# Kernel optimization log

Hardware: AMD Instinct MI355X
Metric: run time of the kernel (lower is better)

The kernel has to match this reference:

```python
import jax, jax.numpy as jnp
import numpy as np


def setup_inputs() -> dict:
    key = jax.random.key(0)
    B, L, C = 32, 1024, 32
    batch_x = jax.random.normal(key, (B, L, C), dtype=jnp.float32)
    return {"batch_x": batch_x, "w": 32}


def reference(batch_x, w):
    # Faithful banded version of dtw_slack: for each timestep t, look at the
    # window [t-w, t+w], compute euclidean distances / n_channels, take the
    # window max, then reduce M = max_t and R2 = sum_t max_t^2 per sample.
    B, L, C = batch_x.shape
    offs = jnp.arange(-w, w + 1)                       # [2w+1]
    t = jnp.arange(L)
    idx = t[:, None] + offs[None, :]                   # [L, 2w+1]
    valid = (idx >= 0) & (idx < L)                     # band edge mask
    idx_c = jnp.clip(idx, 0, L - 1)
    win = batch_x[:, idx_c, :]                         # [B, L, 2w+1, C]
    diff = batch_x[:, :, None, :] - win                # [B, L, 2w+1, C]
    sq = jnp.sum(diff * diff, axis=-1)                 # [B, L, 2w+1]
    # safe sqrt (sqrt(0)=0 exactly, matches torch forward)
    dist = jnp.where(sq > 0, jnp.sqrt(jnp.where(sq > 0, sq, 1.0)), 0.0) / C
    dist = jnp.where(valid[None, :, :], dist, -jnp.inf)
    max_d = jnp.max(dist, axis=2)                      # [B, L]
    M = jnp.max(max_d, axis=1)                         # [B]
    R2 = jnp.sum(max_d * max_d, axis=1)                # [B]
    return (M, R2)
```

## Files before the change

kernel.cpp:

```cpp
#include <hip/hip_runtime.h>
#include <math.h>


#define BB 32
#define LL 1024
#define CC 32
#define WW 32
#define TT 32
#define NROWS (TT + 2*WW)
#define PADH 40
#define NTILES (LL / TT)

typedef __attribute__((ext_vector_type(8))) short bf16x8;
typedef __attribute__((ext_vector_type(4))) float f32x4;

__global__ __launch_bounds__(128)
void sm_main(const float* __restrict__ x, float* __restrict__ ws) {
    const int b    = blockIdx.x;
    const int tile = blockIdx.y;
    const int t0   = tile * TT;
    const int tid  = threadIdx.x;
    const int l    = tid & 63;
    const int w    = tid >> 6;

    __shared__ __align__(16) unsigned short hi[NROWS * PADH];
    __shared__ __align__(16) unsigned short lo[NROWS * PADH];
    __shared__ __align__(16) float nrm_part[NROWS * 8];
    __shared__ float nrm[NROWS];
    __shared__ float redm[8], redr[8];

    const float* xb = x + (size_t)b * (LL * CC);

    #pragma unroll
    for (int k = 0; k < 6; ++k) {
        const int f4 = tid + k * 128;
        const int rr = f4 >> 3;
        const int j  = f4 & 7;
        const int rg = t0 - WW + rr;
        float4 v = make_float4(0.f, 0.f, 0.f, 0.f);
        if ((unsigned)rg < (unsigned)LL)
            v = *reinterpret_cast<const float4*>(xb + rg * CC + j * 4);
        float vv[4] = {v.x, v.y, v.z, v.w};
        unsigned short hb[4], lb[4];
        float s = 0.f;
        #pragma unroll
        for (int e = 0; e < 4; ++e) {
            const float xe = vv[e];
            const unsigned ux = __float_as_uint(xe);
            hb[e] = (unsigned short)(ux >> 16);
            const float hf = __uint_as_float(ux & 0xFFFF0000u);
            const float lf = xe - hf;
            lb[e] = (unsigned short)(__float_as_uint(lf) >> 16);
            s = fmaf(xe, xe, s);
        }
        *reinterpret_cast<ushort4*>(&hi[rr * PADH + j * 4]) = make_ushort4(hb[0], hb[1], hb[2], hb[3]);
        *reinterpret_cast<ushort4*>(&lo[rr * PADH + j * 4]) = make_ushort4(lb[0], lb[1], lb[2], lb[3]);
        nrm_part[f4] = s;
    }
    __syncthreads();

    if (tid < NROWS) {
        const float4* p = reinterpret_cast<const float4*>(&nrm_part[tid * 8]);
        const float4 a = p[0], c = p[1];
        nrm[tid] = ((a.x + a.y) + (a.z + a.w)) + ((c.x + c.y) + (c.z + c.w));
    }
    __syncthreads();

    const int kc = (l >> 4) * 8;
    const int ar = 32 + 16 * w + (l & 15);
    const bf16x8 Ah = *reinterpret_cast<const bf16x8*>(&hi[ar * PADH + kc]);
    const bf16x8 Al = *reinterpret_cast<const bf16x8*>(&lo[ar * PADH + kc]);

    const int col = l & 15;
    float maxsq[4] = {0.f, 0.f, 0.f, 0.f};

    #pragma unroll
    for (int ct = 0; ct < 6; ++ct) {
        const int br = ct * 16 + col;
        const bf16x8 Bh = *reinterpret_cast<const bf16x8*>(&hi[br * PADH + kc]);
        const bf16x8 Bl = *reinterpret_cast<const bf16x8*>(&lo[br * PADH + kc]);
        f32x4 acc = {0.f, 0.f, 0.f, 0.f};
        acc = __builtin_amdgcn_mfma_f32_16x16x32_bf16(Ah, Bh, acc, 0, 0, 0);
        acc = __builtin_amdgcn_mfma_f32_16x16x32_bf16(Ah, Bl, acc, 0, 0, 0);
        acc = __builtin_amdgcn_mfma_f32_16x16x32_bf16(Al, Bh, acc, 0, 0, 0);

        const int r  = br;
        const int rg = t0 - WW + r;
        const float nr = nrm[r];
        #pragma unroll
        for (int i = 0; i < 4; ++i) {
            const int t = 16 * w + (l >> 4) * 4 + i;
            if (r >= t && r <= t + 64 && (unsigned)rg < (unsigned)LL) {
                const float sq = nrm[t + 32] + nr - 2.0f * acc[i];
                maxsq[i] = fmaxf(maxsq[i], sq);
            }
        }
    }

    #pragma unroll
    for (int i = 0; i < 4; ++i) {
        float m = maxsq[i];
        #pragma unroll
        for (int s = 1; s < 16; s <<= 1) m = fmaxf(m, __shfl_xor(m, s));
        maxsq[i] = m;
    }
    if ((l & 15) == 0) {
        float dm = 0.f, r2 = 0.f;
        #pragma unroll
        for (int i = 0; i < 4; ++i) {
            const float d = sqrtf(fmaxf(maxsq[i], 0.f)) * (1.0f / CC);
            dm = fmaxf(dm, d);
            r2 = fmaf(d, d, r2);
        }
        redm[w * 4 + (l >> 4)] = dm;
        redr[w * 4 + (l >> 4)] = r2;
    }
    __syncthreads();

    if (tid == 0) {
        float dm = redm[0], r2 = redr[0];
        #pragma unroll
        for (int g = 1; g < 8; ++g) { dm = fmaxf(dm, redm[g]); r2 += redr[g]; }
        float* slot = ws + (size_t)(b * NTILES + tile) * 2;
        slot[0] = dm;
        slot[1] = r2;
    }
}

__global__ __launch_bounds__(64)
void sm_reduce(const float* __restrict__ ws, float* __restrict__ out) {
    const int b = threadIdx.x;
    if (b < BB) {
        float m = 0.f, r2 = 0.f;
        for (int k = 0; k < NTILES; ++k) {
            m   = fmaxf(m, ws[(size_t)(b * NTILES + k) * 2]);
            r2 +=           ws[(size_t)(b * NTILES + k) * 2 + 1];
        }
        out[b]      = m;
        out[BB + b] = r2;
    }
}

extern "C" void kernel_launch(void* const* d_in, const int* in_sizes, int n_in,
                              void* d_out, int out_size, void* d_ws, size_t ws_size,
                              hipStream_t stream) {
    const float* x  = (const float*)d_in[0];
    float* ws  = (float*)d_ws;
    float* out = (float*)d_out;

    sm_main<<<dim3(BB, NTILES), 128, 0, stream>>>(x, ws);
    sm_reduce<<<1, 64, 0, stream>>>(ws, out);
}
```

Measured before the change: 11.50 us.

## Fuse final reduction into main kernel via last-block atomic counter and double tile size

Doubles the time tile to 64 rows with 256 threads per block, so each block loads 128 rows for 64 outputs and halo reloading drops. Each wave now computes only the 5 column tiles overlapping its band, which removes wasted MFMA work. The separate reduce kernel is replaced by a threadfence-plus-atomic counter, and the last block finishing reduces all per-tile partials. This saves one kernel launch but adds a memset launch and a serialized tail reduction in one block.

After: 25.70 us. 123% more time.

```diff
diff --git a/kernel.cpp b/kernel.cpp
--- a/kernel.cpp
+++ b/kernel.cpp
@@ -6,16 +6,18 @@
 #define LL 1024
 #define CC 32
 #define WW 32
-#define TT 32
+#define TT 64
 #define NROWS (TT + 2*WW)
 #define PADH 40
 #define NTILES (LL / TT)
+#define NBLK (BB * NTILES)
 
 typedef __attribute__((ext_vector_type(8))) short bf16x8;
 typedef __attribute__((ext_vector_type(4))) float f32x4;
 
-__global__ __launch_bounds__(128)
-void sm_main(const float* __restrict__ x, float* __restrict__ ws) {
+__global__ __launch_bounds__(256)
+void sm_fused(const float* __restrict__ x, float* __restrict__ ws,
+              int* __restrict__ cnt, float* __restrict__ out) {
     const int b    = blockIdx.x;
     const int tile = blockIdx.y;
     const int t0   = tile * TT;
@@ -27,13 +29,14 @@
     __shared__ __align__(16) unsigned short lo[NROWS * PADH];
     __shared__ __align__(16) float nrm_part[NROWS * 8];
     __shared__ float nrm[NROWS];
-    __shared__ float redm[8], redr[8];
+    __shared__ float redm[16], redr[16];
+    __shared__ int lastFlag;
 
     const float* xb = x + (size_t)b * (LL * CC);
 
     #pragma unroll
-    for (int k = 0; k < 6; ++k) {
-        const int f4 = tid + k * 128;
+    for (int k = 0; k < 4; ++k) {
+        const int f4 = tid + k * 256;
         const int rr = f4 >> 3;
         const int j  = f4 & 7;
         const int rg = t0 - WW + rr;
@@ -75,8 +78,8 @@
     float maxsq[4] = {0.f, 0.f, 0.f, 0.f};
 
     #pragma unroll
-    for (int ct = 0; ct < 6; ++ct) {
-        const int br = ct * 16 + col;
+    for (int ct = 0; ct < 5; ++ct) {
+        const int br = 16 * w + 16 * ct + col;
         const bf16x8 Bh = *reinterpret_cast<const bf16x8*>(&hi[br * PADH + kc]);
         const bf16x8 Bl = *reinterpret_cast<const bf16x8*>(&lo[br * PADH + kc]);
         f32x4 acc = {0.f, 0.f, 0.f, 0.f};
@@ -84,14 +87,13 @@
         acc = __builtin_amdgcn_mfma_f32_16x16x32_bf16(Ah, Bl, acc, 0, 0, 0);
         acc = __builtin_amdgcn_mfma_f32_16x16x32_bf16(Al, Bh, acc, 0, 0, 0);
 
-        const int r  = br;
-        const int rg = t0 - WW + r;
-        const float nr = nrm[r];
+        const int rg = t0 - WW + br;
+        const float nr = nrm[br];
         #pragma unroll
         for (int i = 0; i < 4; ++i) {
-            const int t = 16 * w + (l >> 4) * 4 + i;
-            if (r >= t && r <= t + 64 && (unsigned)rg < (unsigned)LL) {
-                const float sq = nrm[t + 32] + nr - 2.0f * acc[i];
+            const int ic = 16 * w + (l >> 4) * 4 + i;
+            if (br >= ic && br <= ic + 64 && (unsigned)rg < (unsigned)LL) {
+                const float sq = nrm[ic + 32] + nr - 2.0f * acc[i];
                 maxsq[i] = fmaxf(maxsq[i], sq);
             }
         }
@@ -120,24 +122,33 @@
     if (tid == 0) {
         float dm = redm[0], r2 = redr[0];
         #pragma unroll
-        for (int g = 1; g < 8; ++g) { dm = fmaxf(dm, redm[g]); r2 += redr[g]; }
+        for (int g = 1; g < 16; ++g) { dm = fmaxf(dm, redm[g]); r2 += redr[g]; }
         float* slot = ws + (size_t)(b * NTILES + tile) * 2;
         slot[0] = dm;
         slot[1] = r2;
+        __threadfence();
+        const int old = atomicAdd(cnt, 1);
+        lastFlag = (old == NBLK - 1) ? 1 : 0;
     }
-}
+    __syncthreads();
 
-__global__ __launch_bounds__(64)
-void sm_reduce(const float* __restrict__ ws, float* __restrict__ out) {
-    const int b = threadIdx.x;
-    if (b < BB) {
-        float m = 0.f, r2 = 0.f;
-        for (int k = 0; k < NTILES; ++k) {
-            m   = fmaxf(m, ws[(size_t)(b * NTILES + k) * 2]);
-            r2 +=           ws[(size_t)(b * NTILES + k) * 2 + 1];
+    if (lastFlag) {
+        __threadfence();
+        const int bb = tid >> 3;
+        const int j  = tid & 7;
+        const float* s0 = ws + (size_t)(bb * NTILES + j) * 2;
+        const float* s1 = ws + (size_t)(bb * NTILES + j + 8) * 2;
+        float m  = fmaxf(s0[0], s1[0]);
+        float r2 = s0[1] + s1[1];
+        #pragma unroll
+        for (int s = 1; s < 8; s <<= 1) {
+            m  = fmaxf(m, __shfl_xor(m, s));
+            r2 += __shfl_xor(r2, s);
         }
-        out[b]      = m;
-        out[BB + b] = r2;
+        if (j == 0) {
+            out[bb]      = m;
+            out[BB + bb] = r2;
+        }
     }
 }
 
@@ -146,8 +157,9 @@
                               hipStream_t stream) {
     const float* x  = (const float*)d_in[0];
     float* ws  = (float*)d_ws;
+    int*   cnt = (int*)((char*)d_ws + NBLK * 2 * sizeof(float));
     float* out = (float*)d_out;
 
-    sm_main<<<dim3(BB, NTILES), 128, 0, stream>>>(x, ws);
-    sm_reduce<<<1, 64, 0, stream>>>(ws, out);
+    hipMemsetAsync(cnt, 0, sizeof(int), stream);
+    sm_fused<<<dim3(BB, NTILES), 256, 0, stream>>>(x, ws, cnt, out);
 }
```
